# Optimization experiments

Measured on AMD Instinct MI355X. Metric: run time of the kernel, lower is better.

Reference implementation:

```python
import jax, jax.numpy as jnp
import numpy as np

N = 100_000      # nodes
E = 1_600_000    # edges
D = 128          # hidden_channels
L = 3            # num_layers
G = 5_000        # number of subgraphs (batch ids)
MAXZ = 1_000     # max_z


def setup_inputs() -> dict:
    key = jax.random.key(0)
    ks = jax.random.split(key, 8)
    s = 1.0 / np.sqrt(D)
    return {
        "z": jax.random.randint(ks[0], (N,), 0, MAXZ, dtype=jnp.int32),
        "edge_index": jax.random.randint(ks[1], (2, E), 0, N, dtype=jnp.int32),
        # sorted graph ids, G segments of equal size (each subgraph has >=2 nodes)
        "batch": (jnp.arange(N) * G // N).astype(jnp.int32),
        "z_table": jax.random.normal(ks[2], (MAXZ, D), dtype=jnp.float32) * s,
        "Wl": jax.random.normal(ks[3], (L, D, D), dtype=jnp.float32) * s,
        "bl": jnp.zeros((L, D), jnp.float32),
        "Wr": jax.random.normal(ks[4], (L, D, D), dtype=jnp.float32) * s,
        "W1": jax.random.normal(ks[5], (D, D), dtype=jnp.float32) * s,
        "b1": jnp.zeros((D,), jnp.float32),
        "W2": jax.random.normal(ks[6], (1, D), dtype=jnp.float32) * s,
        "b2": jnp.zeros((1,), jnp.float32),
    }


def reference(z, edge_index, batch, z_table, Wl, bl, Wr, W1, b1, W2, b2):
    src, dst = edge_index[0], edge_index[1]
    x = z_table[z]  # [N, D] z-label embedding (use_feature=False, no node_embedding)

    # in-degree for mean aggregation (shared across layers)
    counts = jax.ops.segment_sum(jnp.ones((E,), x.dtype), dst, num_segments=N)
    inv_deg = 1.0 / jnp.maximum(counts, 1.0)  # [N]

    for l in range(L):
        # SAGEConv: mean-aggregate neighbor features, then lin_l(agg) + lin_r(x)
        agg = jax.ops.segment_sum(x[src], dst, num_segments=N) * inv_deg[:, None]
        x = agg @ Wl[l].T + bl[l] + x @ Wr[l].T
        if l < L - 1:
            x = jax.nn.relu(x)  # dropout is identity in eval mode

    # first node index of each sorted batch segment (np.unique return_index equiv.)
    centers = jnp.searchsorted(batch, jnp.arange(G))  # [G]
    h = x[centers] * x[centers + 1]                   # pairwise center product
    h = jax.nn.relu(h @ W1.T + b1)
    return h @ W2.T + b2  # [G, 1]
```

## Files before the change

### kernel.cpp

```cpp
#include <hip/hip_runtime.h>
#include <hip/hip_bf16.h>
#include <hip/hip_fp16.h>

#define D 128
#define NL 3
#define NODE_SH 8
#define NB_MAX 512
#define BIN_CHUNK 4096

typedef __attribute__((ext_vector_type(8))) short short8;
typedef __attribute__((ext_vector_type(8))) _Float16 half8;
typedef __attribute__((ext_vector_type(4))) float f32x4;

static inline size_t align256(size_t x){ return (x + 255) & ~(size_t)255; }

__global__ __launch_bounds__(256) void k_embed(const int* __restrict__ z, const float* __restrict__ zt,
                                               __half* __restrict__ xh, int N){
    int i = blockIdx.x * blockDim.x + threadIdx.x;
    int n = i >> 5, q = i & 31;
    if (n >= N) return;
    float4 v = *(const float4*)&zt[(size_t)z[n] * D + q * 4];
    __half2 p0 = __floats2half2_rn(v.x, v.y);
    __half2 p1 = __floats2half2_rn(v.z, v.w);
    uint2 u;
    u.x = *reinterpret_cast<unsigned*>(&p0);
    u.y = *reinterpret_cast<unsigned*>(&p1);
    *(uint2*)&xh[(size_t)n * D + q * 4] = u;
}

__global__ __launch_bounds__(256) void k_bcount(const int* __restrict__ dst, int* __restrict__ bcnt,
                                                int E, int NB){
    __shared__ int h[NB_MAX];
    const int t = threadIdx.x;
    for (int b = t; b < NB_MAX; b += 256) h[b] = 0;
    __syncthreads();
    const int stride = gridDim.x * 256;
    for (int e = blockIdx.x * 256 + t; e < E; e += stride)
        atomicAdd(&h[dst[e] >> NODE_SH], 1);
    __syncthreads();
    for (int b = t; b < NB; b += 256){
        int v = h[b];
        if (v) atomicAdd(&bcnt[b], v);
    }
}

__global__ __launch_bounds__(512) void k_bscan(const int* __restrict__ bcnt, int* __restrict__ gbase,
                                               int* __restrict__ gcur, int* __restrict__ offs,
                                               int NB, int N, int E){
    __shared__ int s[512];
    int t = threadIdx.x;
    int v = (t < NB) ? bcnt[t] : 0;
    s[t] = v; __syncthreads();
    for (int st = 1; st < 512; st <<= 1){
        int u = (t >= st) ? s[t - st] : 0;
        __syncthreads();
        s[t] += u;
        __syncthreads();
    }
    if (t < NB){
        int base = s[t] - v;
        gbase[t] = base;
        gcur[t] = base;
    }
    if (t == 0){ gbase[NB] = E; offs[N] = E; }
}

__global__ __launch_bounds__(256) void k_binA(const int* __restrict__ src, const int* __restrict__ dst,
                                              int* __restrict__ gcur, int* __restrict__ ebuf2,
                                              int E, int NB){
    __shared__ int s_hist[NB_MAX];
    __shared__ int s_lofs[NB_MAX];
    __shared__ int s_delta[NB_MAX];
    __shared__ int s_pack[BIN_CHUNK];
    __shared__ int s_gdst[BIN_CHUNK];
    __shared__ int s_scan[256];
    const int t = threadIdx.x;
    const int e0 = blockIdx.x * BIN_CHUNK;
    for (int b = t; b < NB_MAX; b += 256) s_hist[b] = 0;
    __syncthreads();
    int my_pack[16], my_b[16], my_rank[16];
    #pragma unroll
    for (int i = 0; i < 16; ++i){
        int e = e0 + i * 256 + t;
        if (e < E){
            int s = src[e], d = dst[e];
            int b = d >> NODE_SH;
            my_pack[i] = s | ((d & 255) << 17);
            my_b[i] = b;
            my_rank[i] = atomicAdd(&s_hist[b], 1);
        } else my_b[i] = -1;
    }
    __syncthreads();
    int h0 = s_hist[2 * t], h1 = s_hist[2 * t + 1];
    int sum2 = h0 + h1;
    s_scan[t] = sum2;
    __syncthreads();
    for (int st = 1; st < 256; st <<= 1){
        int v = (t >= st) ? s_scan[t - st] : 0;
        __syncthreads();
        s_scan[t] += v;
        __syncthreads();
    }
    int excl = s_scan[t] - sum2;
    s_lofs[2 * t] = excl;
    s_lofs[2 * t + 1] = excl + h0;
    __syncthreads();
    for (int b = t; b < NB; b += 256){
        int h = s_hist[b];
        int base = (h > 0) ? atomicAdd(&gcur[b], h) : 0;
        s_delta[b] = base - s_lofs[b];
    }
    __syncthreads();
    #pragma unroll
    for (int i = 0; i < 16; ++i){
        if (my_b[i] >= 0){
            int j = s_lofs[my_b[i]] + my_rank[i];
            s_pack[j] = my_pack[i];
            s_gdst[j] = j + s_delta[my_b[i]];
        }
    }
    __syncthreads();
    const int cnt = min(BIN_CHUNK, E - e0);
    for (int j = t; j < cnt; j += 256)
        ebuf2[s_gdst[j]] = s_pack[j];
}

__global__ __launch_bounds__(256) void k_binB(const int* __restrict__ ebuf2, const int* __restrict__ gbase,
                                              int* __restrict__ ebuf, int* __restrict__ offs,
                                              float* __restrict__ invdeg, int N){
    __shared__ int cnt[256];
    __shared__ int lcur[256];
    __shared__ int s_scan[256];
    const int b = blockIdx.x, t = threadIdx.x;
    const int n0 = b << NODE_SH;
    const int rs = gbase[b], re = gbase[b + 1];
    cnt[t] = 0;
    __syncthreads();
    for (int i = rs + t; i < re; i += 256)
        atomicAdd(&cnt[ebuf2[i] >> 17], 1);
    __syncthreads();
    const int c = cnt[t];
    s_scan[t] = c;
    __syncthreads();
    for (int st = 1; st < 256; st <<= 1){
        int u = (t >= st) ? s_scan[t - st] : 0;
        __syncthreads();
        s_scan[t] += u;
        __syncthreads();
    }
    const int excl = s_scan[t] - c;
    lcur[t] = rs + excl;
    if (n0 + t < N){
        offs[n0 + t]   = rs + excl;
        invdeg[n0 + t] = 1.0f / (float)max(c, 1);
    }
    __syncthreads();
    for (int i = rs + t; i < re; i += 256){
        int v = ebuf2[i];
        int p = atomicAdd(&lcur[v >> 17], 1);
        ebuf[p] = v & 0x1FFFF;
    }
}

__global__ __launch_bounds__(256) void k_centers(const int* __restrict__ batch, int* __restrict__ centers, int N){
    int n = blockIdx.x * blockDim.x + threadIdx.x;
    if (n < N && (n == 0 || batch[n] != batch[n - 1])) centers[batch[n]] = n;
}

__global__ __launch_bounds__(256) void k_prepW(const float* __restrict__ Wl, const float* __restrict__ Wr,
                                               const float* __restrict__ W1, float* __restrict__ W1T,
                                               __half* __restrict__ WFh, __half* __restrict__ WFl){
    int i = blockIdx.x * blockDim.x + threadIdx.x;
    if (i < NL * 8 * 8 * 64){
        int lane = i & 63;
        int r = i >> 6;
        int fn = r & 7; r >>= 3;
        int ks = r & 7; r >>= 3;
        int l = r;
        int col = fn * 16 + (lane & 15);
        int k0 = ks * 32 + (lane >> 4) * 8;
        __half hh[8], ll[8];
        #pragma unroll
        for (int j = 0; j < 8; ++j){
            int k = k0 + j;
            float w = (k < D) ? Wl[(size_t)l * D * D + col * D + k]
                              : Wr[(size_t)l * D * D + col * D + (k - D)];
            __half h = __float2half(w);
            hh[j] = h;
            ll[j] = __float2half(w - __half2float(h));
        }
        #pragma unroll
        for (int j = 0; j < 8; ++j){
            WFh[(size_t)i * 8 + j] = hh[j];
            WFl[(size_t)i * 8 + j] = ll[j];
        }
    }
    if (i < D * D){ int k = i / D, d = i % D; W1T[i] = W1[d * D + k]; }
}

static __device__ inline void acc_h4(float4& a, uint2 u){
    __half2 h0 = *reinterpret_cast<__half2*>(&u.x);
    __half2 h1 = *reinterpret_cast<__half2*>(&u.y);
    float2 f0 = __half22float2(h0);
    float2 f1 = __half22float2(h1);
    a.x += f0.x; a.y += f0.y; a.z += f1.x; a.w += f1.y;
}

__global__ __launch_bounds__(256) void k_agg(const __half* __restrict__ xh, const int* __restrict__ ebuf,
                                             const int* __restrict__ offs, const float* __restrict__ invdeg,
                                             __half* __restrict__ aggh, int N){
    int node = blockIdx.x * 8 + (threadIdx.x >> 5);
    if (node >= N) return;
    int lane = threadIdx.x & 31;
    int s = offs[node], e = offs[node + 1];
    float4 a0 = make_float4(0.f,0.f,0.f,0.f), a1 = a0, a2 = a0, a3 = a0;
    int i = s;
    for (; i + 4 <= e; i += 4){
        int nb0 = ebuf[i], nb1 = ebuf[i+1], nb2 = ebuf[i+2], nb3 = ebuf[i+3];
        uint2 u0 = *(const uint2*)&xh[(size_t)nb0 * D + lane * 4];
        uint2 u1 = *(const uint2*)&xh[(size_t)nb1 * D + lane * 4];
        uint2 u2 = *(const uint2*)&xh[(size_t)nb2 * D + lane * 4];
        uint2 u3 = *(const uint2*)&xh[(size_t)nb3 * D + lane * 4];
        acc_h4(a0, u0); acc_h4(a1, u1); acc_h4(a2, u2); acc_h4(a3, u3);
    }
    for (; i < e; ++i){
        uint2 u = *(const uint2*)&xh[(size_t)ebuf[i] * D + lane * 4];
        acc_h4(a0, u);
    }
    a0.x += a1.x + a2.x + a3.x;
    a0.y += a1.y + a2.y + a3.y;
    a0.z += a1.z + a2.z + a3.z;
    a0.w += a1.w + a2.w + a3.w;
    float sc = invdeg[node];
    __half2 p0 = __floats2half2_rn(a0.x * sc, a0.y * sc);
    __half2 p1 = __floats2half2_rn(a0.z * sc, a0.w * sc);
    uint2 u;
    u.x = *reinterpret_cast<unsigned*>(&p0);
    u.y = *reinterpret_cast<unsigned*>(&p1);
    *(uint2*)&aggh[(size_t)node * D + lane * 4] = u;
}

template<bool FINAL>
__global__ __launch_bounds__(256) void k_dense_mfma(const __half* __restrict__ Agh, const __half* __restrict__ Xh,
                                                    const __half* __restrict__ WFh, const __half* __restrict__ WFl,
                                                    const float* __restrict__ bias,
                                                    float* __restrict__ Out, __half* __restrict__ XhOut, int N){
    const int wave = threadIdx.x >> 6;
    const int lane = threadIdx.x & 63;
    const int l15  = lane & 15;
    const int kg   = lane >> 4;
    const int rbase = blockIdx.x * 128 + wave * 32;

    f32x4 acc[2][8];
    #pragma unroll
    for (int t = 0; t < 2; ++t)
        #pragma unroll
        for (int fn = 0; fn < 8; ++fn) acc[t][fn] = (f32x4){0.f, 0.f, 0.f, 0.f};

    #pragma unroll
    for (int ks = 0; ks < 8; ++ks){
        const __half* S = (ks < 4) ? Agh : Xh;
        const int ko = (ks & 3) * 32 + kg * 8;
        half8 av[2];
        #pragma unroll
        for (int t = 0; t < 2; ++t){
            int row = rbase + t * 16 + l15;
            row = min(row, N - 1);
            av[t] = *(const half8*)&S[(size_t)row * D + ko];
        }
        #pragma unroll
        for (int fn = 0; fn < 8; ++fn){
            const size_t fo = ((size_t)(ks * 8 + fn) * 64 + lane) * 8;
            const half8 bh = *(const half8*)&WFh[fo];
            const half8 bl = *(const half8*)&WFl[fo];
            #pragma unroll
            for (int t = 0; t < 2; ++t){
                acc[t][fn] = __builtin_amdgcn_mfma_f32_16x16x32_f16(av[t], bh, acc[t][fn], 0, 0, 0);
                acc[t][fn] = __builtin_amdgcn_mfma_f32_16x16x32_f16(av[t], bl, acc[t][fn], 0, 0, 0);
            }
        }
    }
    #pragma unroll
    for (int t = 0; t < 2; ++t){
        const int rb = rbase + t * 16 + (kg << 2);
        #pragma unroll
        for (int fn = 0; fn < 8; ++fn){
            const int col = fn * 16 + l15;
            const float bv = bias[col];
            #pragma unroll
            for (int r = 0; r < 4; ++r){
                const int orow = rb + r;
                if (orow < N){
                    float v = acc[t][fn][r] + bv;
                    if (!FINAL){
                        v = fmaxf(v, 0.f);
                        XhOut[(size_t)orow * D + col] = __float2half(v);
                    } else {
                        Out[(size_t)orow * D + col] = v;
                    }
                }
            }
        }
    }
}

__global__ __launch_bounds__(128) void k_head(const float* __restrict__ x, const int* __restrict__ centers,
                                              const float* __restrict__ W1T, const float* __restrict__ b1,
                                              const float* __restrict__ W2, const float* __restrict__ b2,
                                              float* __restrict__ out){
    __shared__ float hs[D];
    __shared__ float red[D];
    int g = blockIdx.x; int d = threadIdx.x;
    int c = centers[g];
    hs[d] = x[(size_t)c * D + d] * x[(size_t)(c + 1) * D + d];
    __syncthreads();
    float acc = b1[d];
    #pragma unroll 8
    for (int k = 0; k < D; ++k) acc = fmaf(hs[k], W1T[k * D + d], acc);
    acc = fmaxf(acc, 0.f);
    red[d] = acc * W2[d];
    __syncthreads();
    for (int st = 64; st > 0; st >>= 1){
        if (d < st) red[d] += red[d + st];
        __syncthreads();
    }
    if (d == 0) out[g] = red[0] + b2[0];
}

extern "C" void kernel_launch(void* const* d_in, const int* in_sizes, int n_in,
                              void* d_out, int out_size, void* d_ws, size_t ws_size,
                              hipStream_t stream){
    const int*   z     = (const int*)  d_in[0];
    const int*   eidx  = (const int*)  d_in[1];
    const int*   batch = (const int*)  d_in[2];
    const float* zt    = (const float*)d_in[3];
    const float* Wl    = (const float*)d_in[4];
    const float* bl    = (const float*)d_in[5];
    const float* Wr    = (const float*)d_in[6];
    const float* W1    = (const float*)d_in[7];
    const float* b1    = (const float*)d_in[8];
    const float* W2    = (const float*)d_in[9];
    const float* b2    = (const float*)d_in[10];
    float* out = (float*)d_out;

    const int N = in_sizes[0];
    const int E = in_sizes[1] / 2;
    const int G = out_size;
    const int NB = (N + 255) >> NODE_SH;
    const int* src  = eidx;
    const int* dstp = eidx + E;

    char* p = (char*)d_ws;
    auto alloc = [&](size_t bytes){ char* r = p; p += align256(bytes); return r; };
    float*  xf     = (float*)alloc((size_t)N * D * 4);
    __half* aggh   = (__half*)alloc((size_t)N * D * 2);
    __half* xha    = (__half*)alloc((size_t)N * D * 2);
    __half* xhb    = (__half*)alloc((size_t)N * D * 2);
    float* invdeg  = (float*)alloc((size_t)N * 4);
    int*   offs    = (int*)  alloc((size_t)(N + 1) * 4);
    int*   ebuf    = (int*)  alloc((size_t)E * 4);
    int*   ebuf2   = (int*)  alloc((size_t)E * 4);
    int*   centers = (int*)  alloc((size_t)G * 4);
    int*   bcnt    = (int*)  alloc((size_t)NB_MAX * 4);
    int*   gbase   = (int*)  alloc((size_t)(NB_MAX + 1) * 4);
    int*   gcur    = (int*)  alloc((size_t)NB_MAX * 4);
    float* W1T     = (float*)alloc((size_t)D * D * 4);
    __half* WFh    = (__half*)alloc((size_t)NL * 8 * 8 * 64 * 8 * 2);
    __half* WFl    = (__half*)alloc((size_t)NL * 8 * 8 * 64 * 8 * 2);
    (void)ws_size; (void)n_in;

    hipMemsetAsync(bcnt, 0, (size_t)NB_MAX * 4, stream);
    k_embed<<<(N * 32 + 255) / 256, 256, 0, stream>>>(z, zt, xha, N);
    k_bcount<<<512, 256, 0, stream>>>(dstp, bcnt, E, NB);
    k_bscan<<<1, 512, 0, stream>>>(bcnt, gbase, gcur, offs, NB, N, E);
    k_binA<<<(E + BIN_CHUNK - 1) / BIN_CHUNK, 256, 0, stream>>>(src, dstp, gcur, ebuf2, E, NB);
    k_binB<<<NB, 256, 0, stream>>>(ebuf2, gbase, ebuf, offs, invdeg, N);
    k_centers<<<(N + 255) / 256, 256, 0, stream>>>(batch, centers, N);
    k_prepW<<<64, 256, 0, stream>>>(Wl, Wr, W1, W1T, WFh, WFl);

    __half* xhc = xha; __half* xhn = xhb;
    for (int l = 0; l < NL; ++l){
        k_agg<<<(N + 7) / 8, 256, 0, stream>>>(xhc, ebuf, offs, invdeg, aggh, N);
        const __half* wh = WFh + (size_t)l * 8 * 8 * 64 * 8;
        const __half* wl = WFl + (size_t)l * 8 * 8 * 64 * 8;
        if (l < NL - 1)
            k_dense_mfma<false><<<(N + 127) / 128, 256, 0, stream>>>(aggh, xhc, wh, wl, bl + l * D, nullptr, xhn, N);
        else
            k_dense_mfma<true ><<<(N + 127) / 128, 256, 0, stream>>>(aggh, xhc, wh, wl, bl + l * D, xf, nullptr, N);
        __half* th = xhc; xhc = xhn; xhn = th;
    }
    k_head<<<G, 128, 0, stream>>>(xf, centers, W1T, b1, W2, b2, out);
}
```

Before: 499.2 us.

## Fuse neighbor aggregation into the MFMA dense kernel via shared memory

Merges the mean-aggregation kernel into the dense MFMA kernel. Each 64-node block gathers neighbor features into an fp32 shared-memory tile, then feeds it to the MFMA stage with an hi/lo fp16 split, which adds one extra MFMA per fragment. This removes the intermediate agg buffer write/read and one launch per layer, and unrolls the gather to 8 neighbors in flight. The trade-offs are smaller tiles (16 rows per wave, so weight fragments are reused less), extra MFMA work, and a synchronisation between the gather and compute phases that reduces overlap.

```diff
diff --git a/kernel.cpp b/kernel.cpp
--- a/kernel.cpp
+++ b/kernel.cpp
@@ -7,8 +7,8 @@
 #define NODE_SH 8
 #define NB_MAX 512
 #define BIN_CHUNK 4096
-
-typedef __attribute__((ext_vector_type(8))) short short8;
+#define BN 64
+
 typedef __attribute__((ext_vector_type(8))) _Float16 half8;
 typedef __attribute__((ext_vector_type(4))) float f32x4;
 
@@ -206,98 +206,113 @@
     a.x += f0.x; a.y += f0.y; a.z += f1.x; a.w += f1.y;
 }
 
-__global__ __launch_bounds__(256) void k_agg(const __half* __restrict__ xh, const int* __restrict__ ebuf,
-                                             const int* __restrict__ offs, const float* __restrict__ invdeg,
-                                             __half* __restrict__ aggh, int N){
-    int node = blockIdx.x * 8 + (threadIdx.x >> 5);
-    if (node >= N) return;
-    int lane = threadIdx.x & 31;
-    int s = offs[node], e = offs[node + 1];
-    float4 a0 = make_float4(0.f,0.f,0.f,0.f), a1 = a0, a2 = a0, a3 = a0;
-    int i = s;
-    for (; i + 4 <= e; i += 4){
-        int nb0 = ebuf[i], nb1 = ebuf[i+1], nb2 = ebuf[i+2], nb3 = ebuf[i+3];
-        uint2 u0 = *(const uint2*)&xh[(size_t)nb0 * D + lane * 4];
-        uint2 u1 = *(const uint2*)&xh[(size_t)nb1 * D + lane * 4];
-        uint2 u2 = *(const uint2*)&xh[(size_t)nb2 * D + lane * 4];
-        uint2 u3 = *(const uint2*)&xh[(size_t)nb3 * D + lane * 4];
-        acc_h4(a0, u0); acc_h4(a1, u1); acc_h4(a2, u2); acc_h4(a3, u3);
-    }
-    for (; i < e; ++i){
-        uint2 u = *(const uint2*)&xh[(size_t)ebuf[i] * D + lane * 4];
-        acc_h4(a0, u);
-    }
-    a0.x += a1.x + a2.x + a3.x;
-    a0.y += a1.y + a2.y + a3.y;
-    a0.z += a1.z + a2.z + a3.z;
-    a0.w += a1.w + a2.w + a3.w;
-    float sc = invdeg[node];
-    __half2 p0 = __floats2half2_rn(a0.x * sc, a0.y * sc);
-    __half2 p1 = __floats2half2_rn(a0.z * sc, a0.w * sc);
-    uint2 u;
-    u.x = *reinterpret_cast<unsigned*>(&p0);
-    u.y = *reinterpret_cast<unsigned*>(&p1);
-    *(uint2*)&aggh[(size_t)node * D + lane * 4] = u;
-}
-
 template<bool FINAL>
-__global__ __launch_bounds__(256) void k_dense_mfma(const __half* __restrict__ Agh, const __half* __restrict__ Xh,
-                                                    const __half* __restrict__ WFh, const __half* __restrict__ WFl,
-                                                    const float* __restrict__ bias,
-                                                    float* __restrict__ Out, __half* __restrict__ XhOut, int N){
+__global__ __launch_bounds__(256) void k_fused(const __half* __restrict__ Xh,
+                                               const int* __restrict__ ebuf, const int* __restrict__ offs,
+                                               const float* __restrict__ invdeg,
+                                               const __half* __restrict__ WFh, const __half* __restrict__ WFl,
+                                               const float* __restrict__ bias,
+                                               float* __restrict__ Out, __half* __restrict__ XhOut, int N){
+    __shared__ __align__(16) float sA[BN][132];
+    const int base = blockIdx.x * BN;
+
+    {
+        const int hw = threadIdx.x >> 5;
+        const int lane = threadIdx.x & 31;
+        for (int nn = hw; nn < BN; nn += 8){
+            const int node = base + nn;
+            float4 a0 = make_float4(0.f,0.f,0.f,0.f);
+            if (node < N){
+                const int s = offs[node], e = offs[node + 1];
+                float4 a1 = a0, a2 = a0, a3 = a0, a4 = a0, a5 = a0, a6 = a0, a7 = a0;
+                int i = s;
+                for (; i + 8 <= e; i += 8){
+                    int n0 = ebuf[i],   n1 = ebuf[i+1], n2 = ebuf[i+2], n3 = ebuf[i+3];
+                    int n4 = ebuf[i+4], n5 = ebuf[i+5], n6 = ebuf[i+6], n7 = ebuf[i+7];
+                    uint2 u0 = *(const uint2*)&Xh[(size_t)n0 * D + lane * 4];
+                    uint2 u1 = *(const uint2*)&Xh[(size_t)n1 * D + lane * 4];
+                    uint2 u2 = *(const uint2*)&Xh[(size_t)n2 * D + lane * 4];
+                    uint2 u3 = *(const uint2*)&Xh[(size_t)n3 * D + lane * 4];
+                    uint2 u4 = *(const uint2*)&Xh[(size_t)n4 * D + lane * 4];
+                    uint2 u5 = *(const uint2*)&Xh[(size_t)n5 * D + lane * 4];
+                    uint2 u6 = *(const uint2*)&Xh[(size_t)n6 * D + lane * 4];
+                    uint2 u7 = *(const uint2*)&Xh[(size_t)n7 * D + lane * 4];
+                    acc_h4(a0, u0); acc_h4(a1, u1); acc_h4(a2, u2); acc_h4(a3, u3);
+                    acc_h4(a4, u4); acc_h4(a5, u5); acc_h4(a6, u6); acc_h4(a7, u7);
+                }
+                for (; i < e; ++i){
+                    uint2 u = *(const uint2*)&Xh[(size_t)ebuf[i] * D + lane * 4];
+                    acc_h4(a0, u);
+                }
+                a0.x += a1.x + a2.x + a3.x + a4.x + a5.x + a6.x + a7.x;
+                a0.y += a1.y + a2.y + a3.y + a4.y + a5.y + a6.y + a7.y;
+                a0.z += a1.z + a2.z + a3.z + a4.z + a5.z + a6.z + a7.z;
+                a0.w += a1.w + a2.w + a3.w + a4.w + a5.w + a6.w + a7.w;
+                const float sc = invdeg[node];
+                a0.x *= sc; a0.y *= sc; a0.z *= sc; a0.w *= sc;
+            }
+            *(float4*)&sA[nn][lane * 4] = a0;
+        }
+    }
+    __syncthreads();
+
     const int wave = threadIdx.x >> 6;
     const int lane = threadIdx.x & 63;
     const int l15  = lane & 15;
     const int kg   = lane >> 4;
-    const int rbase = blockIdx.x * 128 + wave * 32;
-
-    f32x4 acc[2][8];
+
+    f32x4 acc[8];
     #pragma unroll
-    for (int t = 0; t < 2; ++t)
-        #pragma unroll
-        for (int fn = 0; fn < 8; ++fn) acc[t][fn] = (f32x4){0.f, 0.f, 0.f, 0.f};
+    for (int fn = 0; fn < 8; ++fn) acc[fn] = (f32x4){0.f, 0.f, 0.f, 0.f};
 
     #pragma unroll
     for (int ks = 0; ks < 8; ++ks){
-        const __half* S = (ks < 4) ? Agh : Xh;
         const int ko = (ks & 3) * 32 + kg * 8;
-        half8 av[2];
-        #pragma unroll
-        for (int t = 0; t < 2; ++t){
-            int row = rbase + t * 16 + l15;
-            row = min(row, N - 1);
-            av[t] = *(const half8*)&S[(size_t)row * D + ko];
+        half8 av, al;
+        bool split;
+        if (ks < 4){
+            const int rl = wave * 16 + l15;
+            float4 v0 = *(const float4*)&sA[rl][ko];
+            float4 v1 = *(const float4*)&sA[rl][ko + 4];
+            float f[8] = {v0.x, v0.y, v0.z, v0.w, v1.x, v1.y, v1.z, v1.w};
+            #pragma unroll
+            for (int j = 0; j < 8; ++j){
+                _Float16 h = (_Float16)f[j];
+                av[j] = h;
+                al[j] = (_Float16)(f[j] - (float)h);
+            }
+            split = true;
+        } else {
+            int row = min(base + wave * 16 + l15, N - 1);
+            av = *(const half8*)&Xh[(size_t)row * D + ko];
+            split = false;
         }
         #pragma unroll
         for (int fn = 0; fn < 8; ++fn){
             const size_t fo = ((size_t)(ks * 8 + fn) * 64 + lane) * 8;
             const half8 bh = *(const half8*)&WFh[fo];
             const half8 bl = *(const half8*)&WFl[fo];
-            #pragma unroll
-            for (int t = 0; t < 2; ++t){
-                acc[t][fn] = __builtin_amdgcn_mfma_f32_16x16x32_f16(av[t], bh, acc[t][fn], 0, 0, 0);
-                acc[t][fn] = __builtin_amdgcn_mfma_f32_16x16x32_f16(av[t], bl, acc[t][fn], 0, 0, 0);
-            }
-        }
-    }
+            acc[fn] = __builtin_amdgcn_mfma_f32_16x16x32_f16(av, bh, acc[fn], 0, 0, 0);
+            if (split)
+                acc[fn] = __builtin_amdgcn_mfma_f32_16x16x32_f16(al, bh, acc[fn], 0, 0, 0);
+            acc[fn] = __builtin_amdgcn_mfma_f32_16x16x32_f16(av, bl, acc[fn], 0, 0, 0);
+        }
+    }
+    const int rb = base + wave * 16 + (kg << 2);
     #pragma unroll
-    for (int t = 0; t < 2; ++t){
-        const int rb = rbase + t * 16 + (kg << 2);
+    for (int fn = 0; fn < 8; ++fn){
+        const int col = fn * 16 + l15;
+        const float bv = bias[col];
         #pragma unroll
-        for (int fn = 0; fn < 8; ++fn){
-            const int col = fn * 16 + l15;
-            const float bv = bias[col];
-            #pragma unroll
-            for (int r = 0; r < 4; ++r){
-                const int orow = rb + r;
-                if (orow < N){
-                    float v = acc[t][fn][r] + bv;
-                    if (!FINAL){
-                        v = fmaxf(v, 0.f);
-                        XhOut[(size_t)orow * D + col] = __float2half(v);
-                    } else {
-                        Out[(size_t)orow * D + col] = v;
-                    }
+        for (int r = 0; r < 4; ++r){
+            const int orow = rb + r;
+            if (orow < N){
+                float v = acc[fn][r] + bv;
+                if (!FINAL){
+                    v = fmaxf(v, 0.f);
+                    XhOut[(size_t)orow * D + col] = __float2half(v);
+                } else {
+                    Out[(size_t)orow * D + col] = v;
                 }
             }
         }
@@ -353,7 +368,6 @@
     char* p = (char*)d_ws;
     auto alloc = [&](size_t bytes){ char* r = p; p += align256(bytes); return r; };
     float*  xf     = (float*)alloc((size_t)N * D * 4);
-    __half* aggh   = (__half*)alloc((size_t)N * D * 2);
     __half* xha    = (__half*)alloc((size_t)N * D * 2);
     __half* xhb    = (__half*)alloc((size_t)N * D * 2);
     float* invdeg  = (float*)alloc((size_t)N * 4);
@@ -380,13 +394,12 @@
 
     __half* xhc = xha; __half* xhn = xhb;
     for (int l = 0; l < NL; ++l){
-        k_agg<<<(N + 7) / 8, 256, 0, stream>>>(xhc, ebuf, offs, invdeg, aggh, N);
         const __half* wh = WFh + (size_t)l * 8 * 8 * 64 * 8;
         const __half* wl = WFl + (size_t)l * 8 * 8 * 64 * 8;
         if (l < NL - 1)
-            k_dense_mfma<false><<<(N + 127) / 128, 256, 0, stream>>>(aggh, xhc, wh, wl, bl + l * D, nullptr, xhn, N);
+            k_fused<false><<<(N + BN - 1) / BN, 256, 0, stream>>>(xhc, ebuf, offs, invdeg, wh, wl, bl + l * D, nullptr, xhn, N);
         else
-            k_dense_mfma<true ><<<(N + 127) / 128, 256, 0, stream>>>(aggh, xhc, wh, wl, bl + l * D, xf, nullptr, N);
+            k_fused<true ><<<(N + BN - 1) / BN, 256, 0, stream>>>(xhc, ebuf, offs, invdeg, wh, wl, bl + l * D, xf, nullptr, N);
         __half* th = xhc; xhc = xhn; xhn = th;
     }
     k_head<<<G, 128, 0, stream>>>(xf, centers, W1T, b1, W2, b2, out);
```

Result: slower. 661.0 us (+32.4%).
